# Kernel optimization log

Hardware: AMD Instinct MI355X
Metric: run time of the kernel (lower is better)

## Reference

```python
import jax, jax.numpy as jnp
import numpy as np

D_MODEL = 1024
NUM_HEADS = 16
D_HEAD = 64  # d_q = d_k = d_v
BATCH = 4
SEQ = 2048


def _trunc_normal(key, shape, std):
    # truncated normal in [-3*std, 3*std], matching nn.init.trunc_normal_
    return jax.random.truncated_normal(key, -3.0, 3.0, shape, dtype=jnp.float32) * std


def setup_inputs() -> dict:
    key = jax.random.key(0)
    k_x, k_q, k_k, k_v, k_o = jax.random.split(key, 5)
    hd = NUM_HEADS * D_HEAD
    s_in = np.sqrt(2.0 / (D_MODEL + hd))
    s_out = np.sqrt(2.0 / (hd + D_MODEL))
    return {
        "in_features": jax.random.normal(k_x, (BATCH, SEQ, D_MODEL), dtype=jnp.float32),
        "w_q": _trunc_normal(k_q, (hd, D_MODEL), s_in),
        "w_k": _trunc_normal(k_k, (hd, D_MODEL), s_in),
        "w_v": _trunc_normal(k_v, (hd, D_MODEL), s_in),
        "w_o": _trunc_normal(k_o, (D_MODEL, hd), s_out),
    }


def reference(in_features, w_q, w_k, w_v, w_o):
    B, S, D = in_features.shape
    H, Dh = NUM_HEADS, D_HEAD
    # QKV projections (weight stored as [out, in])
    q = jnp.einsum('od,bsd->bso', w_q, in_features).reshape(B, S, H, Dh).transpose(0, 2, 1, 3)
    k = jnp.einsum('od,bsd->bso', w_k, in_features).reshape(B, S, H, Dh).transpose(0, 2, 1, 3)
    v = jnp.einsum('od,bsd->bso', w_v, in_features).reshape(B, S, H, Dh).transpose(0, 2, 1, 3)
    # scaled dot-product attention with dense causal mask (as in source)
    att = jnp.einsum('bhqd,bhkd->bhqk', q, k) / jnp.sqrt(jnp.float32(Dh)).astype(q.dtype)
    causal = jnp.tril(jnp.ones((S, S), dtype=bool))
    att = jnp.where(causal, att, -jnp.inf)
    att = jax.nn.softmax(att, axis=-1)
    out = jnp.einsum('bhqk,bhkd->bhqd', att, v)  # [B,H,S,Dh]
    out = out.transpose(0, 2, 1, 3).reshape(B, S, H * Dh)
    return jnp.einsum('od,bsd->bso', w_o, out)
```

## Files before the change

kernel.cpp:

```cpp
#include <hip/hip_runtime.h>
#include <stdint.h>

#define D_MODEL 1024
#define NHEADS  16
#define DHEAD   64
#define BATCH   4
#define SEQ     2048
#define MTOT    (BATCH*SEQ)

typedef unsigned short u16;
typedef uint32_t u32;
typedef __bf16 bf16x8 __attribute__((ext_vector_type(8)));
typedef float  f32x4  __attribute__((ext_vector_type(4)));
typedef float  f32x16 __attribute__((ext_vector_type(16)));
typedef u16    u16x8  __attribute__((ext_vector_type(8)));
typedef u16    u16x4  __attribute__((ext_vector_type(4)));
typedef u32    u32x4  __attribute__((ext_vector_type(4)));

__device__ __forceinline__ u16 f2bf(float f) {
  uint32_t u = __builtin_bit_cast(uint32_t, f);
  u += 0x7fff + ((u >> 16) & 1);
  return (u16)(u >> 16);
}

__device__ __forceinline__ void gll16(const u16* g, u16* lds) {
  __builtin_amdgcn_global_load_lds(
      (__attribute__((address_space(1))) void*)(g),
      (__attribute__((address_space(3))) void*)(lds), 16, 0, 0);
}

__global__ void cvtk(const float4* __restrict__ in, u16x4* __restrict__ out, int n4) {
  const int i = blockIdx.x * blockDim.x + threadIdx.x;
  if (i < n4) {
    const float4 f = in[i];
    u16x4 h;
    h[0] = f2bf(f.x); h[1] = f2bf(f.y); h[2] = f2bf(f.z); h[3] = f2bf(f.w);
    out[i] = h;
  }
}

__global__ void cvtk4(const float4* __restrict__ a, const float4* __restrict__ b,
                      const float4* __restrict__ c, const float4* __restrict__ d,
                      u16x4* __restrict__ out, int n4) {
  const int i = blockIdx.x * blockDim.x + threadIdx.x;
  if (i >= n4) return;
  const float4* src = (blockIdx.y == 0) ? a : (blockIdx.y == 1) ? b
                    : (blockIdx.y == 2) ? c : d;
  const float4 f = src[i];
  u16x4 h;
  h[0] = f2bf(f.x); h[1] = f2bf(f.y); h[2] = f2bf(f.z); h[3] = f2bf(f.w);
  out[(size_t)blockIdx.y * n4 + i] = h;
}

#define QS 8192
#define BARS() __builtin_amdgcn_s_barrier()
#define LGKM0() do { asm volatile("s_waitcnt lgkmcnt(0)" ::: "memory"); \
                     __builtin_amdgcn_sched_barrier(0); } while (0)

#define QP3 28672

#define Q3_ASTG(roff, t_, dstoff) do {                                            \
    gll16(pA + (size_t)(roff)*1024 + (t_)*64,      qsm + (dstoff) + w*512);       \
    gll16(pA + (size_t)((roff)+64)*1024 + (t_)*64, qsm + (dstoff) + w*512 + 4096);\
  } while (0)

#define Q3_BSTG(t_, dstoff) do {                                                  \
    gll16(pB + (size_t)0*1024  + (t_)*64, qsm + (dstoff) + w*1536);               \
    gll16(pB + (size_t)8*1024  + (t_)*64, qsm + (dstoff) + w*1536 + 512);         \
    gll16(pB + (size_t)16*1024 + (t_)*64, qsm + (dstoff) + w*1536 + 1024);        \
  } while (0)

#define Q3_READS_P1() do {                                                        \
    _Pragma("unroll")                                                             \
    for (int mf = 0; mf < 8; ++mf) {                                              \
      af0[mf] = *(const bf16x8*)&sA[(mf*16 + r15)*64 + cs0];                      \
      af1[mf] = *(const bf16x8*)&sA[(mf*16 + r15)*64 + cs1];                      \
    }                                                                             \
    _Pragma("unroll")                                                             \
    for (int nf = 0; nf < 3; ++nf)                                                \
      bq[nf] = *(const bf16x8*)&sB[(brow + nf*16 + r15)*64 + cs0];                \
  } while (0)

#define Q3_READS_P2() do {                                                        \
    _Pragma("unroll")                                                             \
    for (int nf = 0; nf < 3; ++nf)                                                \
      bq[nf] = *(const bf16x8*)&sB[(brow + nf*16 + r15)*64 + cs1];                \
  } while (0)

#define Q3_MM(AF) do {                                                            \
    __builtin_amdgcn_s_setprio(1);                                                \
    _Pragma("unroll")                                                             \
    for (int mf = 0; mf < 8; ++mf)                                                \
      _Pragma("unroll")                                                           \
      for (int nf = 0; nf < 3; ++nf)                                              \
        acc[mf][nf] = __builtin_amdgcn_mfma_f32_16x16x32_bf16(AF[mf], bq[nf],     \
                                                              acc[mf][nf], 0,0,0);\
    __builtin_amdgcn_s_setprio(0);                                                \
  } while (0)

__global__ __launch_bounds__(512, 2) void gemm_qkv192(
    const u16* __restrict__ A, const u16* __restrict__ Bw, u16* __restrict__ Out)
{
  extern __shared__ u16 qsm[];
  const int tid = threadIdx.x;
  const int w = tid >> 6, l = tid & 63;
  const int wm = w >> 2, wn = w & 3;
  const int bid = blockIdx.x;
  const int wg = (bid & 7) * 64 + (bid >> 3);
  const int m0 = (wg >> 4) * 256, n0 = (wg & 15) * 192;

  const int sc8 = ((l & 7) ^ ((l >> 3) & 7)) * 8;
  const u16* pA = A  + (size_t)(m0 + 8*w  + (l >> 3)) * 1024 + sc8;
  const u16* pB = Bw + (size_t)(n0 + 24*w + (l >> 3)) * 1024 + sc8;

  const int r15 = l & 15;
  const int cs0 = (((l >> 4) + 0) ^ (l & 7)) * 8;
  const int cs1 = (((l >> 4) + 4) ^ (l & 7)) * 8;
  const int brow = wn * 48;

  f32x4 acc[8][3];
  #pragma unroll
  for (int i = 0; i < 8; ++i)
    #pragma unroll
    for (int j = 0; j < 3; ++j)
      acc[i][j] = f32x4{0.f, 0.f, 0.f, 0.f};

  Q3_ASTG(0,   0, 0);
  Q3_ASTG(128, 0, 8192);
  Q3_BSTG(0, 16384);
  Q3_ASTG(0,   1, QP3 + 0);
  Q3_ASTG(128, 1, QP3 + 8192);
  asm volatile("s_waitcnt vmcnt(4)" ::: "memory");
  BARS();
  __builtin_amdgcn_sched_barrier(0);

  #pragma unroll 2
  for (int t = 0; t < 14; ++t) {
    const int p = t & 1, po = p ^ 1;
    const u16* sA = qsm + (size_t)p*QP3 + (size_t)wm*8192;
    const u16* sB = qsm + (size_t)p*QP3 + 16384;
    bf16x8 af0[8], af1[8], bq[3];
    Q3_READS_P1();
    Q3_BSTG(t+1, po*QP3 + 16384);
    BARS(); LGKM0();
    Q3_MM(af0);
    BARS();
    Q3_READS_P2();
    Q3_ASTG(0,   t+2, p*QP3 + 0);
    Q3_ASTG(128, t+2, p*QP3 + 8192);
    BARS(); LGKM0();
    Q3_MM(af1);
    asm volatile("s_waitcnt vmcnt(4)" ::: "memory");
    BARS();
    __builtin_amdgcn_sched_barrier(0);
  }

  {
    const u16* sA = qsm + (size_t)wm*8192;
    const u16* sB = qsm + 16384;
    bf16x8 af0[8], af1[8], bq[3];
    Q3_READS_P1();
    Q3_BSTG(15, QP3 + 16384);
    BARS(); LGKM0();
    Q3_MM(af0);
    BARS();
    Q3_READS_P2();
    BARS(); LGKM0();
    Q3_MM(af1);
    asm volatile("s_waitcnt vmcnt(0)" ::: "memory");
    BARS();
    __builtin_amdgcn_sched_barrier(0);
  }
  {
    const u16* sA = qsm + (size_t)QP3 + (size_t)wm*8192;
    const u16* sB = qsm + (size_t)QP3 + 16384;
    bf16x8 af0[8], af1[8], bq[3];
    Q3_READS_P1();
    Q3_MM(af0);
    Q3_READS_P2();
    Q3_MM(af1);
  }

  const float qs = 0.125f * 1.44269504088896f;
  const int g = l >> 4, c15 = l & 15;
  #pragma unroll
  for (int mf = 0; mf < 8; ++mf) {
    #pragma unroll
    for (int nf = 0; nf < 3; ++nf) {
      #pragma unroll
      for (int j = 0; j < 4; ++j) {
        const int row = m0 + wm*128 + mf*16 + g*4 + j;
        const int col = n0 + wn*48 + nf*16 + c15;
        const int z = col >> 10;
        const int wi = col & 1023;
        const float scale = (z == 0) ? qs : 1.0f;
        const int b = row >> 11, sq = row & (SEQ-1);
        const int h = wi >> 6, dh = wi & (DHEAD-1);
        Out[(size_t)z * MTOT * D_MODEL
            + ((size_t)(b*NHEADS + h) * SEQ + sq) * DHEAD + dh] =
            f2bf(acc[mf][nf][j] * scale);
      }
    }
  }
}

#undef Q3_ASTG
#undef Q3_BSTG
#undef Q3_READS_P1
#undef Q3_READS_P2
#undef Q3_MM

#define OSTG(pbase, roff, t_, slot_) do {                                       \
    gll16((pbase) + (size_t)(roff)*1024 + (t_)*64,      osm + (slot_)*QS + w*512);        \
    gll16((pbase) + (size_t)((roff)+64)*1024 + (t_)*64, osm + (slot_)*QS + w*512 + 4096); \
  } while (0)

#define OREADS_P1() do {                                                        \
    _Pragma("unroll")                                                           \
    for (int mf = 0; mf < 8; ++mf) {                                            \
      af0[mf] = *(const bf16x8*)&sA[(mf*16 + r15)*64 + cs0];                    \
      af1[mf] = *(const bf16x8*)&sA[(mf*16 + r15)*64 + cs1];                    \
    }                                                                           \
    _Pragma("unroll")                                                           \
    for (int nf = 0; nf < 2; ++nf)                                              \
      bq[nf] = *(const bf16x8*)&sB[(brow + nf*16 + r15)*64 + cs0];              \
  } while (0)

#define OREADS_P2() do {                                                        \
    _Pragma("unroll")                                                           \
    for (int nf = 0; nf < 2; ++nf)                                              \
      bq[nf] = *(const bf16x8*)&sB[(brow + nf*16 + r15)*64 + cs1];              \
  } while (0)

#define OMM(AF) do {                                                            \
    __builtin_amdgcn_s_setprio(1);                                              \
    _Pragma("unroll")                                                           \
    for (int mf = 0; mf < 8; ++mf) {                                            \
      acc[mf][0] = __builtin_amdgcn_mfma_f32_16x16x32_bf16(AF[mf], bq[0],       \
                                                           acc[mf][0], 0,0,0);  \
      acc[mf][1] = __builtin_amdgcn_mfma_f32_16x16x32_bf16(AF[mf], bq[1],       \
                                                           acc[mf][1], 0,0,0);  \
    }                                                                           \
    __builtin_amdgcn_s_setprio(0);                                              \
  } while (0)

__global__ __launch_bounds__(512, 2) void gemm_o8p(
    const u16* __restrict__ A, const u16* __restrict__ Bw, float* __restrict__ Out)
{
  extern __shared__ u16 osm[];
  const int tid = threadIdx.x;
  const int w = tid >> 6, l = tid & 63;
  const int wm = w >> 2, wn = w & 3;
  const int bid = blockIdx.x;
  const int wg = (bid & 7) * 32 + (bid >> 3);
  const int m0 = (wg >> 3) * 256, n0 = (wg & 7) * 128;

  const int sr  = 8*w + (l >> 3);
  const int sc8 = ((l & 7) ^ ((l >> 3) & 7)) * 8;
  const u16* pA = A  + (size_t)(m0 + sr) * 1024 + sc8;
  const u16* pB = Bw + (size_t)(n0 + sr) * 1024 + sc8;

  const int r15 = l & 15;
  const int cs0 = (((l >> 4) + 0) ^ (l & 7)) * 8;
  const int cs1 = (((l >> 4) + 4) ^ (l & 7)) * 8;
  const int brow = wn * 32;

  f32x4 acc[8][2];
  #pragma unroll
  for (int i = 0; i < 8; ++i) {
    acc[i][0] = f32x4{0.f, 0.f, 0.f, 0.f};
    acc[i][1] = f32x4{0.f, 0.f, 0.f, 0.f};
  }

  OSTG(pA, 0,   0, 0);
  OSTG(pA, 128, 0, 1);
  OSTG(pB, 0,   0, 2);
  OSTG(pA, 0,   1, 3);
  OSTG(pA, 128, 1, 4);
  asm volatile("s_waitcnt vmcnt(4)" ::: "memory");
  BARS();
  __builtin_amdgcn_sched_barrier(0);

  #pragma unroll 2
  for (int t = 0; t < 14; ++t) {
    const int p = t & 1, po = p ^ 1;
    const u16* sA = osm + (size_t)(p*3 + wm) * QS;
    const u16* sB = osm + (size_t)(p*3 + 2) * QS;
    bf16x8 af0[8], af1[8], bq[2];
    OREADS_P1();
    OSTG(pB, 0, t+1, po*3 + 2);
    BARS(); LGKM0();
    OMM(af0);
    BARS();
    OREADS_P2();
    OSTG(pA, 0,   t+2, p*3 + 0);
    OSTG(pA, 128, t+2, p*3 + 1);
    BARS(); LGKM0();
    OMM(af1);
    asm volatile("s_waitcnt vmcnt(4)" ::: "memory");
    BARS();
    __builtin_amdgcn_sched_barrier(0);
  }

  {
    const u16* sA = osm + (size_t)(0*3 + wm) * QS;
    const u16* sB = osm + (size_t)(0*3 + 2) * QS;
    bf16x8 af0[8], af1[8], bq[2];
    OREADS_P1();
    OSTG(pB, 0, 15, 1*3 + 2);
    BARS(); LGKM0();
    OMM(af0);
    BARS();
    OREADS_P2();
    BARS(); LGKM0();
    OMM(af1);
    asm volatile("s_waitcnt vmcnt(0)" ::: "memory");
    BARS();
    __builtin_amdgcn_sched_barrier(0);
  }
  {
    const u16* sA = osm + (size_t)(1*3 + wm) * QS;
    const u16* sB = osm + (size_t)(1*3 + 2) * QS;
    bf16x8 af0[8], af1[8], bq[2];
    OREADS_P1();
    OMM(af0);
    OREADS_P2();
    OMM(af1);
  }

  const int g = l >> 4, c15 = l & 15;
  #pragma unroll
  for (int mf = 0; mf < 8; ++mf) {
    #pragma unroll
    for (int nf = 0; nf < 2; ++nf) {
      #pragma unroll
      for (int j = 0; j < 4; ++j) {
        const int row = m0 + wm*128 + mf*16 + g*4 + j;
        const int col = n0 + wn*32 + nf*16 + c15;
        Out[(size_t)row * D_MODEL + col] = acc[mf][nf][j];
      }
    }
  }
}

#undef OSTG
#undef OREADS_P1
#undef OREADS_P2
#undef OMM

__launch_bounds__(512, 2)
__global__ void attn6_k(const u16* __restrict__ Qb, const u16* __restrict__ Kb_,
                        const u16* __restrict__ Vb_, u16* __restrict__ Oa)
{
  const int tid = threadIdx.x;
  const int w = tid >> 6, l = tid & 63;
  const int q5 = l & 31, hi = l >> 5;
  const int r = blockIdx.x;
  const int bh = (r & 7) * 8 + ((r >> 3) & 7);
  const int pairi = r >> 6;
  const int b = bh >> 4, h = bh & 15;
  const size_t base = (size_t)bh * SEQ * DHEAD;
  const u16* Qg = Qb + base;
  const u16* Kg = Kb_ + base;
  const u16* Vg = Vb_ + base;

  __shared__ __align__(16) u16 smem[32768];

  const int kc = tid & 7, rp = tid >> 3;
  const int vsub = rp >> 5;
  const int rp5 = rp & 31;
  int vIdx32[8];
  #pragma unroll
  for (int e = 0; e < 8; ++e)
    vIdx32[e] = vsub*2048 + (8*kc + e)*32 + ((((rp5 >> 2) ^ kc ^ e) & 7) << 2) + (rp5 & 3);

  const int kr8 = l >> 3;
  const int kkv = 8*w + kr8;
  const int kdc = (l & 7) ^ kr8 ^ w;

  for (int half = 0; half < 2; ++half) {
    const int tq = half ? (7 - pairi) : pairi;
    const int q0w = tq*256 + 32*w;
    const int ntk = (tq + 1) * 2;
    const int ntw = (q0w >> 7) + 1;

    bf16x8 qf[4];
    #pragma unroll
    for (int s = 0; s < 4; ++s)
      qf[s] = *(const bf16x8*)(Qg + (size_t)(q0w + q5)*DHEAD + 16*s + 8*hi);

    f32x16 c0 = {}, c1 = {};
    float mrun = -1e30f, lrun = 0.f;

    {
      #pragma unroll
      for (int h2 = 0; h2 < 2; ++h2)
        gll16(Kg + (size_t)(64*h2 + kkv)*DHEAD + kdc*8, smem + h2*4096 + w*512);
      const u16x8 v0 = *(const u16x8*)(Vg + (size_t)(2*rp)*DHEAD + kc*8);
      const u16x8 v1 = *(const u16x8*)(Vg + (size_t)(2*rp + 1)*DHEAD + kc*8);
      u32* Vd = (u32*)(smem + 16384);
      #pragma unroll
      for (int e = 0; e < 8; ++e)
        Vd[vIdx32[e]] = (u32)v0[e] | ((u32)v1[e] << 16);
    }
    __syncthreads();

    for (int t = 0; t < ntk; ++t) {
      const int cur = t & 1;
      const bool pf = (t + 1 < ntk);
      u16x8 v0, v1;
      if (pf) {
        const int kv1 = (t + 1) * 128;
        v0 = *(const u16x8*)(Vg + (size_t)(kv1 + 2*rp)*DHEAD + kc*8);
        v1 = *(const u16x8*)(Vg + (size_t)(kv1 + 2*rp + 1)*DHEAD + kc*8);
        #pragma unroll
        for (int h2 = 0; h2 < 2; ++h2)
          gll16(Kg + (size_t)(kv1 + 64*h2 + kkv)*DHEAD + kdc*8,
                smem + (cur^1)*8192 + h2*4096 + w*512);
      }

      if (t < ntw) {
        const u16* Kb = smem + cur*8192;
        const u16* Vv = smem + 16384 + cur*8192;

        f32x16 st[4] = {{}, {}, {}, {}};
        __builtin_amdgcn_s_setprio(1);
        #pragma unroll
        for (int kbg = 0; kbg < 4; ++kbg) {
          #pragma unroll
          for (int s = 0; s < 4; ++s) {
            const int slot = ((2*s + hi) ^ (l & 7) ^ ((4*(kbg & 1)) & 7) ^ (q5 >> 3)) & 7;
            const bf16x8 kf = *(const bf16x8*)(Kb + (kbg >> 1)*4096
                                               + ((kbg & 1)*32 + q5)*64 + slot*8);
            st[kbg] = __builtin_amdgcn_mfma_f32_32x32x16_bf16(kf, qf[s], st[kbg], 0, 0, 0);
          }
        }
        __builtin_amdgcn_s_setprio(0);

        if (t == ntw - 1) {
          const int kv0 = t * 128;
          #pragma unroll
          for (int kbg = 0; kbg < 4; ++kbg)
            #pragma unroll
            for (int rr = 0; rr < 16; ++rr) {
              const int kvg = kv0 + 32*kbg + (rr & 3) + 8*(rr >> 2) + 4*hi;
              if (kvg > q0w + q5) st[kbg][rr] = -1e30f;
            }
        }

        float mx = -1e30f;
        #pragma unroll
        for (int kbg = 0; kbg < 4; ++kbg)
          #pragma unroll
          for (int rr = 0; rr < 16; ++rr) mx = fmaxf(mx, st[kbg][rr]);
        mx = fmaxf(mx, __shfl_xor(mx, 32));
        float alpha = 1.0f;
        if (!__all(mx <= mrun + 8.0f)) {
          const float mnew = fmaxf(mrun, mx);
          alpha = __builtin_amdgcn_exp2f(mrun - mnew);
          mrun = mnew;
          #pragma unroll
          for (int rr = 0; rr < 16; ++rr) { c0[rr] *= alpha; c1[rr] *= alpha; }
        }
        float rs = 0.f;
        #pragma unroll
        for (int kbg = 0; kbg < 4; ++kbg)
          #pragma unroll
          for (int rr = 0; rr < 16; ++rr) {
            const float pe = __builtin_amdgcn_exp2f(st[kbg][rr] - mrun);
            st[kbg][rr] = pe;
            rs += pe;
          }
        rs += __shfl_xor(rs, 32);
        lrun = lrun * alpha + rs;

        bf16x8 pb[8];
        #pragma unroll
        for (int kbg = 0; kbg < 4; ++kbg) {
          u32 pw[8];
          #pragma unroll
          for (int i = 0; i < 8; ++i) {
            u32 t0;
            asm("v_cvt_pk_bf16_f32 %0, %1, %2"
                : "=v"(t0) : "v"(st[kbg][2*i]), "v"(st[kbg][2*i+1]));
            pw[i] = t0;
          }
          asm("v_permlane32_swap_b32 %0, %1" : "+v"(pw[0]), "+v"(pw[2]));
          asm("v_permlane32_swap_b32 %0, %1" : "+v"(pw[1]), "+v"(pw[3]));
          asm("v_permlane32_swap_b32 %0, %1" : "+v"(pw[4]), "+v"(pw[6]));
          asm("v_permlane32_swap_b32 %0, %1" : "+v"(pw[5]), "+v"(pw[7]));
          pb[2*kbg]   = __builtin_bit_cast(bf16x8, u32x4{pw[0], pw[1], pw[2], pw[3]});
          pb[2*kbg+1] = __builtin_bit_cast(bf16x8, u32x4{pw[4], pw[5], pw[6], pw[7]});
        }

        __builtin_amdgcn_s_setprio(1);
        #pragma unroll
        for (int h2 = 0; h2 < 2; ++h2) {
          #pragma unroll
          for (int s = 0; s < 4; ++s) {
            {
              const int slot = ((2*s + hi) ^ (l & 7) ^ (q5 >> 3)) & 7;
              const bf16x8 vf = *(const bf16x8*)(Vv + h2*4096 + q5*64 + slot*8);
              c0 = __builtin_amdgcn_mfma_f32_32x32x16_bf16(vf, pb[4*h2 + s], c0, 0, 0, 0);
            }
            {
              const int slot = ((2*s + hi) ^ (l & 7) ^ 4 ^ (q5 >> 3)) & 7;
              const bf16x8 vf = *(const bf16x8*)(Vv + h2*4096 + (32 + q5)*64 + slot*8);
              c1 = __builtin_amdgcn_mfma_f32_32x32x16_bf16(vf, pb[4*h2 + s], c1, 0, 0, 0);
            }
          }
        }
        __builtin_amdgcn_s_setprio(0);
      }

      if (pf) {
        u32* Vd = (u32*)(smem + 16384) + (cur^1)*4096;
        #pragma unroll
        for (int e = 0; e < 8; ++e)
          Vd[vIdx32[e]] = (u32)v0[e] | ((u32)v1[e] << 16);
      }
      __syncthreads();
    }

    const float linv = __builtin_amdgcn_rcpf(lrun);
    #pragma unroll
    for (int Ab = 0; Ab < 2; ++Ab)
      #pragma unroll
      for (int rr = 0; rr < 16; ++rr) {
        const int d = 32*Ab + (rr & 3) + 8*(rr >> 2) + 4*hi;
        smem[w*2048 + q5*64 + (((d >> 3) ^ (q5 & 7)) & 7)*8 + (d & 7)] =
            f2bf((Ab ? c1[rr] : c0[rr]) * linv);
      }
    __syncthreads();
    #pragma unroll
    for (int cc = 0; cc < 4; ++cc) {
      const int dchunk = 4*hi + cc;
      const u16x8 vv = *(const u16x8*)&smem[w*2048 + q5*64 + ((dchunk ^ (q5 & 7)) & 7)*8];
      *(u16x8*)(Oa + (size_t)(b*SEQ + q0w + q5)*D_MODEL + h*DHEAD + 32*hi + 8*cc) = vv;
    }
    __syncthreads();
  }
}

extern "C" void kernel_launch(void* const* d_in, const int* in_sizes, int n_in,
                              void* d_out, int out_size, void* d_ws, size_t ws_size,
                              hipStream_t stream) {
  const float* X  = (const float*)d_in[0];
  const float* Wq = (const float*)d_in[1];
  const float* Wk = (const float*)d_in[2];
  const float* Wv = (const float*)d_in[3];
  const float* Wo = (const float*)d_in[4];

  u16* xb  = (u16*)d_ws;
  u16* wqb = xb  + (size_t)MTOT*D_MODEL;
  u16* wkb = wqb + (size_t)D_MODEL*D_MODEL;
  u16* wvb = wkb + (size_t)D_MODEL*D_MODEL;
  u16* wob = wvb + (size_t)D_MODEL*D_MODEL;
  u16* qkv = wob + (size_t)D_MODEL*D_MODEL;
  u16* att = qkv + (size_t)3*MTOT*D_MODEL;

  (void)hipFuncSetAttribute((const void*)gemm_qkv192,
                            hipFuncAttributeMaxDynamicSharedMemorySize, 114688);
  (void)hipFuncSetAttribute((const void*)gemm_o8p,
                            hipFuncAttributeMaxDynamicSharedMemorySize, 98304);

  const int nx4 = MTOT*D_MODEL/4;
  const int nw4 = D_MODEL*D_MODEL/4;
  cvtk<<<nx4/256, 256, 0, stream>>>((const float4*)X, (u16x4*)xb, nx4);
  dim3 gc(nw4/256, 4, 1);
  cvtk4<<<gc, 256, 0, stream>>>((const float4*)Wq, (const float4*)Wk,
                                (const float4*)Wv, (const float4*)Wo,
                                (u16x4*)wqb, nw4);

  gemm_qkv192<<<512, 512, 114688, stream>>>(xb, wqb, qkv);

  attn6_k<<<256, 512, 0, stream>>>(qkv, qkv + (size_t)MTOT*D_MODEL,
                                   qkv + (size_t)2*MTOT*D_MODEL, att);

  gemm_o8p<<<256, 512, 98304, stream>>>(att, wob, (float*)d_out);
}
```

Before: 146.6 us.

## Fuse fp32-to-bf16 input conversion into the QKV GEMM A-tile staging

Result: slower. 170.7 us (+16.4%).

```diff
diff --git a/kernel.cpp b/kernel.cpp
--- a/kernel.cpp
+++ b/kernel.cpp
@@ -15,6 +15,7 @@
 typedef float  f32x16 __attribute__((ext_vector_type(16)));
 typedef u16    u16x8  __attribute__((ext_vector_type(8)));
 typedef u16    u16x4  __attribute__((ext_vector_type(4)));
+typedef u32    u32x2  __attribute__((ext_vector_type(2)));
 typedef u32    u32x4  __attribute__((ext_vector_type(4)));
 
 __device__ __forceinline__ u16 f2bf(float f) {
@@ -27,16 +28,6 @@
   __builtin_amdgcn_global_load_lds(
       (__attribute__((address_space(1))) void*)(g),
       (__attribute__((address_space(3))) void*)(lds), 16, 0, 0);
-}
-
-__global__ void cvtk(const float4* __restrict__ in, u16x4* __restrict__ out, int n4) {
-  const int i = blockIdx.x * blockDim.x + threadIdx.x;
-  if (i < n4) {
-    const float4 f = in[i];
-    u16x4 h;
-    h[0] = f2bf(f.x); h[1] = f2bf(f.y); h[2] = f2bf(f.z); h[3] = f2bf(f.w);
-    out[i] = h;
-  }
 }
 
 __global__ void cvtk4(const float4* __restrict__ a, const float4* __restrict__ b,
@@ -59,9 +50,27 @@
 
 #define QP3 28672
 
-#define Q3_ASTG(roff, t_, dstoff) do {                                            \
-    gll16(pA + (size_t)(roff)*1024 + (t_)*64,      qsm + (dstoff) + w*512);       \
-    gll16(pA + (size_t)((roff)+64)*1024 + (t_)*64, qsm + (dstoff) + w*512 + 4096);\
+#define QF_AISSUE(t_) do {                                                        \
+    _Pragma("unroll")                                                             \
+    for (int j = 0; j < 8; ++j) {                                                 \
+      const int rr_ = j*32 + w*4 + (l >> 4);                                      \
+      araw[j] = *(const float4*)(A32 + (size_t)(m0 + rr_)*1024 + (t_)*64 + (l & 15)*4); \
+    }                                                                             \
+  } while (0)
+
+#define QF_AWRITE(poff) do {                                                      \
+    _Pragma("unroll")                                                             \
+    for (int j = 0; j < 8; ++j) {                                                 \
+      const int rr_ = j*32 + w*4 + (l >> 4);                                      \
+      u32 c0_, c1_;                                                               \
+      asm("v_cvt_pk_bf16_f32 %0, %1, %2" : "=v"(c0_) : "v"(araw[j].x), "v"(araw[j].y)); \
+      asm("v_cvt_pk_bf16_f32 %0, %1, %2" : "=v"(c1_) : "v"(araw[j].z), "v"(araw[j].w)); \
+      const int pic_ = l & 15;                                                    \
+      const int c_ = pic_ >> 1, hf_ = pic_ & 1;                                   \
+      const int off_ = ((rr_ & 128) ? 8192 : 0) + (rr_ & 127)*64                  \
+                       + ((c_ ^ (rr_ & 7)) << 3) + hf_*4;                         \
+      *(u32x2*)&qsm[(poff) + off_] = u32x2{c0_, c1_};                             \
+    }                                                                             \
   } while (0)
 
 #define Q3_BSTG(t_, dstoff) do {                                                  \
@@ -98,8 +107,8 @@
     __builtin_amdgcn_s_setprio(0);                                                \
   } while (0)
 
-__global__ __launch_bounds__(512, 2) void gemm_qkv192(
-    const u16* __restrict__ A, const u16* __restrict__ Bw, u16* __restrict__ Out)
+__global__ __launch_bounds__(512, 2) void gemm_qkvf(
+    const float* __restrict__ A32, const u16* __restrict__ Bw, u16* __restrict__ Out)
 {
   extern __shared__ u16 qsm[];
   const int tid = threadIdx.x;
@@ -110,7 +119,6 @@
   const int m0 = (wg >> 4) * 256, n0 = (wg & 15) * 192;
 
   const int sc8 = ((l & 7) ^ ((l >> 3) & 7)) * 8;
-  const u16* pA = A  + (size_t)(m0 + 8*w  + (l >> 3)) * 1024 + sc8;
   const u16* pB = Bw + (size_t)(n0 + 24*w + (l >> 3)) * 1024 + sc8;
 
   const int r15 = l & 15;
@@ -125,14 +133,16 @@
     for (int j = 0; j < 3; ++j)
       acc[i][j] = f32x4{0.f, 0.f, 0.f, 0.f};
 
-  Q3_ASTG(0,   0, 0);
-  Q3_ASTG(128, 0, 8192);
+  float4 araw[8];
+
+  QF_AISSUE(0);
+  QF_AWRITE(0);
+  QF_AISSUE(1);
+  QF_AWRITE(QP3);
   Q3_BSTG(0, 16384);
-  Q3_ASTG(0,   1, QP3 + 0);
-  Q3_ASTG(128, 1, QP3 + 8192);
-  asm volatile("s_waitcnt vmcnt(4)" ::: "memory");
+  asm volatile("s_waitcnt vmcnt(0)" ::: "memory");
   BARS();
-  __builtin_amdgcn_sched_barrier(0);
+  LGKM0();
 
   #pragma unroll 2
   for (int t = 0; t < 14; ++t) {
@@ -141,16 +151,16 @@
     const u16* sB = qsm + (size_t)p*QP3 + 16384;
     bf16x8 af0[8], af1[8], bq[3];
     Q3_READS_P1();
+    QF_AISSUE(t+2);
     Q3_BSTG(t+1, po*QP3 + 16384);
     BARS(); LGKM0();
     Q3_MM(af0);
     BARS();
     Q3_READS_P2();
-    Q3_ASTG(0,   t+2, p*QP3 + 0);
-    Q3_ASTG(128, t+2, p*QP3 + 8192);
+    QF_AWRITE(p*QP3);
     BARS(); LGKM0();
     Q3_MM(af1);
-    asm volatile("s_waitcnt vmcnt(4)" ::: "memory");
+    asm volatile("s_waitcnt vmcnt(0)" ::: "memory");
     BARS();
     __builtin_amdgcn_sched_barrier(0);
   }
@@ -204,7 +214,8 @@
   }
 }
 
-#undef Q3_ASTG
+#undef QF_AISSUE
+#undef QF_AWRITE
 #undef Q3_BSTG
 #undef Q3_READS_P1
 #undef Q3_READS_P2
@@ -551,28 +562,23 @@
   const float* Wv = (const float*)d_in[3];
   const float* Wo = (const float*)d_in[4];
 
-  u16* xb  = (u16*)d_ws;
-  u16* wqb = xb  + (size_t)MTOT*D_MODEL;
-  u16* wkb = wqb + (size_t)D_MODEL*D_MODEL;
-  u16* wvb = wkb + (size_t)D_MODEL*D_MODEL;
-  u16* wob = wvb + (size_t)D_MODEL*D_MODEL;
-  u16* qkv = wob + (size_t)D_MODEL*D_MODEL;
+  u16* wqb = (u16*)d_ws;
+  u16* wob = wqb + (size_t)3*D_MODEL*D_MODEL;
+  u16* qkv = wqb + (size_t)4*D_MODEL*D_MODEL;
   u16* att = qkv + (size_t)3*MTOT*D_MODEL;
 
-  (void)hipFuncSetAttribute((const void*)gemm_qkv192,
+  (void)hipFuncSetAttribute((const void*)gemm_qkvf,
                             hipFuncAttributeMaxDynamicSharedMemorySize, 114688);
   (void)hipFuncSetAttribute((const void*)gemm_o8p,
                             hipFuncAttributeMaxDynamicSharedMemorySize, 98304);
 
-  const int nx4 = MTOT*D_MODEL/4;
   const int nw4 = D_MODEL*D_MODEL/4;
-  cvtk<<<nx4/256, 256, 0, stream>>>((const float4*)X, (u16x4*)xb, nx4);
   dim3 gc(nw4/256, 4, 1);
   cvtk4<<<gc, 256, 0, stream>>>((const float4*)Wq, (const float4*)Wk,
                                 (const float4*)Wv, (const float4*)Wo,
                                 (u16x4*)wqb, nw4);
 
-  gemm_qkv192<<<512, 512, 114688, stream>>>(xb, wqb, qkv);
+  gemm_qkvf<<<512, 512, 114688, stream>>>(X, wqb, qkv);
 
   attn6_k<<<256, 512, 0, stream>>>(qkv, qkv + (size_t)MTOT*D_MODEL,
                                    qkv + (size_t)2*MTOT*D_MODEL, att);
```
